# Kernel tuning notes

Measured on AMD Instinct MI355X. Metric: run time of the kernel, lower is better.

Reference implementation:

```python
import jax, jax.numpy as jnp
import numpy as np

B, T, H, IN, OUT = 256, 1024, 512, 2, 2


def setup_inputs() -> dict:
    key = jax.random.key(0)
    ks = jax.random.split(key, 12)
    s = 1.0 / np.sqrt(H)
    return {
        "X0": jax.random.normal(ks[0], (B, OUT), jnp.float32),
        "V": jax.random.normal(ks[1], (B, T, IN), jnp.float32),
        # GRU params (torch layout: gates ordered r, z, n)
        "W_ih": jax.random.uniform(ks[2], (3 * H, IN), jnp.float32, -s, s),
        "W_hh": jax.random.uniform(ks[3], (3 * H, H), jnp.float32, -s, s),
        "b_ih": jax.random.uniform(ks[4], (3 * H,), jnp.float32, -s, s),
        "b_hh": jax.random.uniform(ks[5], (3 * H,), jnp.float32, -s, s),
        # attention MLP: Linear(OUT+IN, H//2) -> ReLU -> Linear(H//2, OUT) -> Softmax
        "Wa1": jax.random.uniform(ks[6], (H // 2, OUT + IN), jnp.float32, -s, s),
        "ba1": jax.random.uniform(ks[7], (H // 2,), jnp.float32, -s, s),
        "Wa2": jax.random.uniform(ks[8], (OUT, H // 2), jnp.float32, -s, s),
        "ba2": jax.random.uniform(ks[9], (OUT,), jnp.float32, -s, s),
        # residual layer: Linear(H, OUT)
        "Wr": jax.random.uniform(ks[10], (OUT, H), jnp.float32, -s, s),
        "br": jax.random.uniform(ks[11], (OUT,), jnp.float32, -s, s),
    }


def _forward(X0, V, W_ih, W_hh, b_ih, b_hh, Wa1, ba1, Wa2, ba2, Wr, br):
    # ---- GRU over time (batch_first input, h0 = 0) ----
    # Precompute input projections for all steps: [B, T, 3H]
    gx_all = jnp.einsum('bti,gi->btg', V, W_ih) + b_ih
    gx_tm = jnp.swapaxes(gx_all, 0, 1)  # [T, B, 3H]

    def gru_step(h, gx):
        gh = h @ W_hh.T + b_hh  # [B, 3H]
        r = jax.nn.sigmoid(gx[:, :H] + gh[:, :H])
        z = jax.nn.sigmoid(gx[:, H:2 * H] + gh[:, H:2 * H])
        n = jnp.tanh(gx[:, 2 * H:] + r * gh[:, 2 * H:])
        h_new = (1.0 - z) * n + z * h
        return h_new, h_new

    h0 = jnp.zeros((V.shape[0], H), V.dtype)
    _, h_seq = jax.lax.scan(gru_step, h0, gx_tm)  # [T, B, H]

    # residual_raw = residual_layer(h_t), precomputed for all t: [T, B, OUT]
    res_all = jnp.einsum('tbh,oh->tbo', h_seq, Wr) + br

    v_tm = jnp.swapaxes(V, 0, 1)  # [T, B, IN]; IN == OUT so slice is identity

    def corr_step(x_prev, inp):
        v_t, res_t = inp
        att_in = jnp.concatenate([x_prev, v_t[:, :OUT]], axis=-1)  # [B, OUT+IN]
        hid = jax.nn.relu(att_in @ Wa1.T + ba1)
        aw = jax.nn.softmax(hid @ Wa2.T + ba2, axis=-1)  # [B, OUT]
        x_t = x_prev + v_t[:, :OUT] + aw * res_t
        return x_t, x_t

    _, x_seq = jax.lax.scan(corr_step, X0, (v_tm, res_all))  # [T, B, OUT]
    return jnp.swapaxes(x_seq, 0, 1)  # [B, T, OUT]


def reference(X0, V, W_ih, W_hh, b_ih, b_hh, Wa1, ba1, Wa2, ba2, Wr, br):
    return _forward(X0, V, W_ih, W_hh, b_ih, b_hh, Wa1, ba1, Wa2, ba2, Wr, br)
```

## Files before the change

kernel.cpp:

```cpp
#include <hip/hip_runtime.h>


typedef short bf16x8 __attribute__((ext_vector_type(8)));
typedef float f32x4  __attribute__((ext_vector_type(4)));
typedef unsigned u32x4 __attribute__((ext_vector_type(4)));

__device__ __forceinline__ unsigned f2bf(float f) {
  unsigned u = __builtin_bit_cast(unsigned, f);
  return (u + 0x7fffu + ((u >> 16) & 1u)) >> 16;
}

#define KSTEP(kt, areg) \
  acc0 = __builtin_amdgcn_mfma_f32_16x16x32_bf16(areg, wf0[kt], acc0, 0, 0, 0); \
  acc1 = __builtin_amdgcn_mfma_f32_16x16x32_bf16(areg, wf1[kt], acc1, 0, 0, 0); \
  acc2 = __builtin_amdgcn_mfma_f32_16x16x32_bf16(areg, wf2[kt], acc2, 0, 0, 0);

#define PUBU(off, val) \
  asm volatile("global_store_dwordx4 %0, %1, off offset:" #off " sc1" \
               :: "v"(pp), "v"(val) : "memory")

__global__ void __launch_bounds__(256, 1) gru_phase1(
    const float* __restrict__ V, const float* __restrict__ W_ih,
    const float* __restrict__ W_hh, const float* __restrict__ b_ih,
    const float* __restrict__ b_hh, const float* __restrict__ Wr,
    float* __restrict__ res_part,
    char* __restrict__ hbuf)
{
  const int tid  = threadIdx.x;
  const int w    = tid >> 6;
  const int lane = tid & 63;
  const int cl   = lane & 15;
  const int hi4  = lane >> 4;
  const int g    = blockIdx.x & 15;
  const int p    = (blockIdx.x >> 4) & 7;

  __shared__ short hs[2][16][512];
  __shared__ float rscratch[4][16][2];
  char* lds = (char*)hs;

  const int c = p * 64 + w * 16 + cl;

  const float wir0 = W_ih[c * 2 + 0],          wir1 = W_ih[c * 2 + 1];
  const float wiz0 = W_ih[(512 + c) * 2 + 0],  wiz1 = W_ih[(512 + c) * 2 + 1];
  const float win0 = W_ih[(1024 + c) * 2 + 0], win1 = W_ih[(1024 + c) * 2 + 1];
  const float bsr = b_ih[c] + b_hh[c];
  const float bsz = b_ih[512 + c] + b_hh[512 + c];
  const float bin = b_ih[1024 + c];
  const float bhn = b_hh[1024 + c];
  const float wr0 = Wr[c], wr1 = Wr[512 + c];

  bf16x8 wf0[16], wf1[16], wf2[16];
  #pragma unroll
  for (int gt = 0; gt < 3; ++gt) {
    const float* src = W_hh + ((size_t)(gt * 512 + c)) * 512 + hi4 * 8;
    #pragma unroll
    for (int kt = 0; kt < 16; ++kt) {
      float4 x = *reinterpret_cast<const float4*>(src + kt * 32);
      float4 y = *reinterpret_cast<const float4*>(src + kt * 32 + 4);
      bf16x8 t;
      t[0] = (short)f2bf(x.x); t[1] = (short)f2bf(x.y);
      t[2] = (short)f2bf(x.z); t[3] = (short)f2bf(x.w);
      t[4] = (short)f2bf(y.x); t[5] = (short)f2bf(y.y);
      t[6] = (short)f2bf(y.z); t[7] = (short)f2bf(y.w);
      if (gt == 0) wf0[kt] = t; else if (gt == 1) wf1[kt] = t; else wf2[kt] = t;
    }
  }

  for (int i = tid; i < 8192; i += 256) ((unsigned*)lds)[i] = 0;
  __syncthreads();

  const int urow = tid >> 4, ucol = tid & 15;
  const unsigned roff = (unsigned)(urow * 256 + ucol * 16);

  float h[4] = {0.f, 0.f, 0.f, 0.f};

  for (int s = 0; s < 1024; ++s) {
    float2 vv[4];
    #pragma unroll
    for (int j = 0; j < 4; ++j)
      vv[j] = *reinterpret_cast<const float2*>(
          &V[((size_t)(g * 16 + hi4 * 4 + j) * 1024 + (size_t)s) * 2]);

    f32x4 acc0 = {0.f,0.f,0.f,0.f}, acc1 = {0.f,0.f,0.f,0.f}, acc2 = {0.f,0.f,0.f,0.f};
    if (s > 0) {
      const char* ab = lds + (s & 1) * 16384 + cl * 1024;
      const unsigned sw = (unsigned)((cl & 7) << 4);
      #pragma unroll
      for (int kb = 0; kb < 4; ++kb) {
        bf16x8 a0 = *(const bf16x8*)(ab + (((kb * 4 + 0) * 64 + hi4 * 16) ^ sw));
        bf16x8 a1 = *(const bf16x8*)(ab + (((kb * 4 + 1) * 64 + hi4 * 16) ^ sw));
        bf16x8 a2 = *(const bf16x8*)(ab + (((kb * 4 + 2) * 64 + hi4 * 16) ^ sw));
        bf16x8 a3 = *(const bf16x8*)(ab + (((kb * 4 + 3) * 64 + hi4 * 16) ^ sw));
        KSTEP(kb * 4 + 0, a0) KSTEP(kb * 4 + 1, a1)
        KSTEP(kb * 4 + 2, a2) KSTEP(kb * 4 + 3, a3)
      }
    }

    float hn_[4];
    #pragma unroll
    for (int j = 0; j < 4; ++j) {
      float pr = acc0[j] + bsr + wir0 * vv[j].x + wir1 * vv[j].y;
      float pz = acc1[j] + bsz + wiz0 * vv[j].x + wiz1 * vv[j].y;
      float rg = 1.f / (1.f + __expf(-pr));
      float zg = 1.f / (1.f + __expf(-pz));
      float pn = win0 * vv[j].x + win1 * vv[j].y + bin + rg * (acc2[j] + bhn);
      pn = fminf(fmaxf(pn, -30.f), 30.f);
      float e2 = __expf(2.f * pn);
      float tg = (e2 - 1.f) / (e2 + 1.f);
      hn_[j] = (1.f - zg) * tg + zg * h[j];
      h[j] = hn_[j];
    }

    unsigned pk[4];
    #pragma unroll
    for (int j = 0; j < 4; ++j) {
      float o = __shfl_xor(hn_[j], 1);
      pk[j] = f2bf(hn_[j]) | (f2bf(o) << 16);
    }

    {
      unsigned q[4];
      #pragma unroll
      for (int j = 0; j < 4; ++j) q[j] = __shfl_xor(pk[j], 2);
      if (!(cl & 3)) {
        char* pp = hbuf + (size_t)(s & 1) * 524288 + (size_t)(g * 8 + p) * 4096
                 + (unsigned)(hi4 * 4) * 256u + (unsigned)((w * 16 + cl) >> 2) * 16u;
        u32x4 v0, v1, v2, v3;
        v0.x = pk[0]; v0.y = q[0]; v0.z = (unsigned)(s + 1); v0.w = 0u;
        v1.x = pk[1]; v1.y = q[1]; v1.z = (unsigned)(s + 1); v1.w = 0u;
        v2.x = pk[2]; v2.y = q[2]; v2.z = (unsigned)(s + 1); v2.w = 0u;
        v3.x = pk[3]; v3.y = q[3]; v3.z = (unsigned)(s + 1); v3.w = 0u;
        PUBU(0, v0); PUBU(256, v1); PUBU(512, v2); PUBU(768, v3);
      }
    }

    if (!(cl & 1)) {
      char* wb = lds + ((s + 1) & 1) * 16384;
      const unsigned bc = (unsigned)(2 * c);
      #pragma unroll
      for (int j = 0; j < 4; ++j) {
        const unsigned row = (unsigned)(hi4 * 4 + j);
        *(unsigned*)(wb + row * 1024 + (bc ^ ((row & 7) << 4))) = pk[j];
      }
    }

    {
      float p0[4], p1[4];
      #pragma unroll
      for (int j = 0; j < 4; ++j) { p0[j] = wr0 * hn_[j]; p1[j] = wr1 * hn_[j]; }
      #pragma unroll
      for (int m = 1; m < 16; m <<= 1) {
        #pragma unroll
        for (int j = 0; j < 4; ++j) {
          p0[j] += __shfl_xor(p0[j], m);
          p1[j] += __shfl_xor(p1[j], m);
        }
      }
      if (cl == 0) {
        #pragma unroll
        for (int j = 0; j < 4; ++j) {
          rscratch[w][hi4 * 4 + j][0] = p0[j];
          rscratch[w][hi4 * 4 + j][1] = p1[j];
        }
      }
    }
    __syncthreads();

    if (tid < 16) {
      float r0 = rscratch[0][tid][0] + rscratch[1][tid][0] +
                 rscratch[2][tid][0] + rscratch[3][tid][0];
      float r1 = rscratch[0][tid][1] + rscratch[1][tid][1] +
                 rscratch[2][tid][1] + rscratch[3][tid][1];
      float2 val; val.x = r0; val.y = r1;
      *reinterpret_cast<float2*>(
          &res_part[(((size_t)s * 256 + g * 16 + tid) * 8 + p) * 2]) = val;
    }

    if (s < 1023) {
      char* wb = lds + ((s + 1) & 1) * 16384;
      const unsigned want = (unsigned)(s + 1);
      const char* sbase = hbuf + (size_t)(s & 1) * 524288 + (size_t)(g * 8) * 4096 + roff;
      u32x4 u0, u1, u2, u3, u4, u5, u6;
      unsigned pend = 0x7f;
      #define RP(r) ((p + (r) + 1) & 7)
      #define ISSUE(r, ureg) \
        if (pend & (1u << (r))) { \
          const char* src = sbase + RP(r) * 4096; \
          asm volatile("global_load_dwordx4 %0, %1, off sc1" \
                       : "=v"(ureg) : "v"(src) : "memory"); \
        }
      #define HARVEST(r, ureg) \
        if ((pend & (1u << (r))) && ureg.z == want) { \
          const unsigned bc = (unsigned)(RP(r) * 128 + ucol * 8); \
          uint2 pay; pay.x = ureg.x; pay.y = ureg.y; \
          *(uint2*)(wb + (unsigned)urow * 1024 + \
                    (bc ^ (((unsigned)urow & 7) << 4))) = pay; \
          pend &= ~(1u << (r)); \
        }
      int gd = 0;
      while (pend) {
        ISSUE(0, u0) ISSUE(1, u1) ISSUE(2, u2) ISSUE(3, u3)
        ISSUE(4, u4) ISSUE(5, u5) ISSUE(6, u6)
        asm volatile("s_waitcnt vmcnt(0)" ::: "memory");
        HARVEST(0, u0) HARVEST(1, u1) HARVEST(2, u2) HARVEST(3, u3)
        HARVEST(4, u4) HARVEST(5, u5) HARVEST(6, u6)
        if (++gd > (1 << 14)) break;
      }
      #undef RP
      #undef ISSUE
      #undef HARVEST
    }
    __syncthreads();
  }
}

__global__ void __launch_bounds__(256) corr_phase2(
    const float* __restrict__ X0,
    const float* __restrict__ V,
    const float* __restrict__ Wa1,
    const float* __restrict__ ba1,
    const float* __restrict__ Wa2,
    const float* __restrict__ ba2,
    const float* __restrict__ br,
    const float* __restrict__ res_part,
    float* __restrict__ out)
{
  const int tid = threadIdx.x;
  const int wv = tid >> 6;
  const int lane = tid & 63;
  const int b = blockIdx.x * 4 + wv;

  float w1[4][4], bb1[4], w20[4], w21[4];
  #pragma unroll
  for (int q = 0; q < 4; q++) {
    const int h = lane * 4 + q;
    #pragma unroll
    for (int c = 0; c < 4; c++) w1[q][c] = Wa1[h * 4 + c];
    bb1[q] = ba1[h];
    w20[q] = Wa2[h];
    w21[q] = Wa2[256 + h];
  }
  const float c20 = ba2[0], c21 = ba2[1];
  const float br0 = br[0], br1 = br[1];
  float x0 = X0[b * 2], x1 = X0[b * 2 + 1];

  for (int c = 0; c < 16; c++) {
    const int tl = c * 64 + lane;
    const float2 vvl = *reinterpret_cast<const float2*>(&V[(b * 1024 + tl) * 2]);
    const float4* rp = reinterpret_cast<const float4*>(
        &res_part[((size_t)tl * 256 + b) * 16]);
    float4 q0 = rp[0], q1 = rp[1], q2 = rp[2], q3 = rp[3];
    float rr0 = (q0.x + q0.z) + (q1.x + q1.z) + (q2.x + q2.z) + (q3.x + q3.z);
    float rr1 = (q0.y + q0.w) + (q1.y + q1.w) + (q2.y + q2.w) + (q3.y + q3.w);
    float sx = 0.f, sy = 0.f;
    for (int k = 0; k < 64; k++) {
      const float v0 = __shfl(vvl.x, k);
      const float v1 = __shfl(vvl.y, k);
      const float r0 = __shfl(rr0, k) + br0;
      const float r1 = __shfl(rr1, k) + br1;
      float l0 = 0.f, l1 = 0.f;
      #pragma unroll
      for (int q = 0; q < 4; q++) {
        float hq = w1[q][0] * x0 + w1[q][1] * x1 + w1[q][2] * v0 + w1[q][3] * v1 + bb1[q];
        hq = fmaxf(hq, 0.f);
        l0 += w20[q] * hq;
        l1 += w21[q] * hq;
      }
      #pragma unroll
      for (int m = 1; m < 64; m <<= 1) {
        l0 += __shfl_xor(l0, m);
        l1 += __shfl_xor(l1, m);
      }
      l0 += c20; l1 += c21;
      const float mx = fmaxf(l0, l1);
      const float e0 = __expf(l0 - mx), e1 = __expf(l1 - mx);
      const float inv = 1.f / (e0 + e1);
      x0 += v0 + (e0 * inv) * r0;
      x1 += v1 + (e1 * inv) * r1;
      if (k == lane) { sx = x0; sy = x1; }
    }
    float2 o; o.x = sx; o.y = sy;
    *reinterpret_cast<float2*>(&out[(b * 1024 + c * 64 + lane) * 2]) = o;
  }
}

extern "C" void kernel_launch(void* const* d_in, const int* in_sizes, int n_in,
                              void* d_out, int out_size, void* d_ws, size_t ws_size,
                              hipStream_t stream) {
  const float* X0   = (const float*)d_in[0];
  const float* V    = (const float*)d_in[1];
  const float* W_ih = (const float*)d_in[2];
  const float* W_hh = (const float*)d_in[3];
  const float* b_ih = (const float*)d_in[4];
  const float* b_hh = (const float*)d_in[5];
  const float* Wa1  = (const float*)d_in[6];
  const float* ba1  = (const float*)d_in[7];
  const float* Wa2  = (const float*)d_in[8];
  const float* ba2  = (const float*)d_in[9];
  const float* Wr   = (const float*)d_in[10];
  const float* br   = (const float*)d_in[11];
  float* out = (float*)d_out;

  char* ws = (char*)d_ws;
  char*  hbuf     = ws;
  float* res_part = (float*)(ws + 1024 * 1024);
  hipMemsetAsync(hbuf, 0, 1024 * 1024, stream);

  hipLaunchKernelGGL(gru_phase1, dim3(128), dim3(256), 0, stream,
                     V, W_ih, W_hh, b_ih, b_hh, Wr, res_part, hbuf);
  hipLaunchKernelGGL(corr_phase2, dim3(64), dim3(256), 0, stream,
                     X0, V, Wa1, ba1, Wa2, ba2, br, res_part, out);
}
```

Measured before the change: 3.889 ms.

## Process two batch groups per GRU block and halve the grid

Each phase-1 block now handles two batch groups with the same register-resident W_hh slice, doubling LDS buffers and scratch, and launches 64 blocks instead of 128. Per-step compute and the two groups' global h exchanges are done back-to-back within one block. This aims to amortise the per-step barrier and latency overhead over more work and cut the number of polling blocks, at the cost of longer per-step critical path per block.

```diff
diff --git a/kernel.cpp b/kernel.cpp
--- a/kernel.cpp
+++ b/kernel.cpp
@@ -31,11 +31,12 @@
   const int lane = tid & 63;
   const int cl   = lane & 15;
   const int hi4  = lane >> 4;
-  const int g    = blockIdx.x & 15;
-  const int p    = (blockIdx.x >> 4) & 7;
-
-  __shared__ short hs[2][16][512];
-  __shared__ float rscratch[4][16][2];
+  const int pr_  = blockIdx.x & 7;
+  const int p    = blockIdx.x >> 3;
+  const int gA   = pr_ * 2, gB = gA + 1;
+
+  __shared__ short hs[2][2][16][512];
+  __shared__ float rsc[2][4][16][2];
   char* lds = (char*)hs;
 
   const int c = p * 64 + w * 16 + cl;
@@ -66,15 +67,16 @@
     }
   }
 
-  for (int i = tid; i < 8192; i += 256) ((unsigned*)lds)[i] = 0;
+  for (int i = tid; i < 16384; i += 256) ((unsigned*)lds)[i] = 0;
   __syncthreads();
 
   const int urow = tid >> 4, ucol = tid & 15;
   const unsigned roff = (unsigned)(urow * 256 + ucol * 16);
 
-  float h[4] = {0.f, 0.f, 0.f, 0.f};
-
-  for (int s = 0; s < 1024; ++s) {
+  float hA[4] = {0.f, 0.f, 0.f, 0.f};
+  float hB[4] = {0.f, 0.f, 0.f, 0.f};
+
+  auto process = [&](int s, int sub, int g, float* h) {
     float2 vv[4];
     #pragma unroll
     for (int j = 0; j < 4; ++j)
@@ -83,7 +85,7 @@
 
     f32x4 acc0 = {0.f,0.f,0.f,0.f}, acc1 = {0.f,0.f,0.f,0.f}, acc2 = {0.f,0.f,0.f,0.f};
     if (s > 0) {
-      const char* ab = lds + (s & 1) * 16384 + cl * 1024;
+      const char* ab = lds + (s & 1) * 32768 + sub * 16384 + cl * 1024;
       const unsigned sw = (unsigned)((cl & 7) << 4);
       #pragma unroll
       for (int kb = 0; kb < 4; ++kb) {
@@ -99,9 +101,9 @@
     float hn_[4];
     #pragma unroll
     for (int j = 0; j < 4; ++j) {
-      float pr = acc0[j] + bsr + wir0 * vv[j].x + wir1 * vv[j].y;
-      float pz = acc1[j] + bsz + wiz0 * vv[j].x + wiz1 * vv[j].y;
-      float rg = 1.f / (1.f + __expf(-pr));
+      float prr = acc0[j] + bsr + wir0 * vv[j].x + wir1 * vv[j].y;
+      float pz  = acc1[j] + bsz + wiz0 * vv[j].x + wiz1 * vv[j].y;
+      float rg = 1.f / (1.f + __expf(-prr));
       float zg = 1.f / (1.f + __expf(-pz));
       float pn = win0 * vv[j].x + win1 * vv[j].y + bin + rg * (acc2[j] + bhn);
       pn = fminf(fmaxf(pn, -30.f), 30.f);
@@ -135,7 +137,7 @@
     }
 
     if (!(cl & 1)) {
-      char* wb = lds + ((s + 1) & 1) * 16384;
+      char* wb = lds + ((s + 1) & 1) * 32768 + sub * 16384;
       const unsigned bc = (unsigned)(2 * c);
       #pragma unroll
       for (int j = 0; j < 4; ++j) {
@@ -159,56 +161,70 @@
       if (cl == 0) {
         #pragma unroll
         for (int j = 0; j < 4; ++j) {
-          rscratch[w][hi4 * 4 + j][0] = p0[j];
-          rscratch[w][hi4 * 4 + j][1] = p1[j];
+          rsc[sub][w][hi4 * 4 + j][0] = p0[j];
+          rsc[sub][w][hi4 * 4 + j][1] = p1[j];
         }
       }
     }
+  };
+
+  auto consume = [&](int s, int sub, int g) {
+    char* wb = lds + ((s + 1) & 1) * 32768 + sub * 16384;
+    const unsigned want = (unsigned)(s + 1);
+    const char* sbase = hbuf + (size_t)(s & 1) * 524288 + (size_t)(g * 8) * 4096 + roff;
+    u32x4 u0, u1, u2, u3, u4, u5, u6;
+    unsigned pend = 0x7f;
+    #define RP(r) ((p + (r) + 1) & 7)
+    #define ISSUE(r, ureg) \
+      if (pend & (1u << (r))) { \
+        const char* src = sbase + RP(r) * 4096; \
+        asm volatile("global_load_dwordx4 %0, %1, off sc1" \
+                     : "=v"(ureg) : "v"(src) : "memory"); \
+      }
+    #define HARVEST(r, ureg) \
+      if ((pend & (1u << (r))) && ureg.z == want) { \
+        const unsigned bc = (unsigned)(RP(r) * 128 + ucol * 8); \
+        uint2 pay; pay.x = ureg.x; pay.y = ureg.y; \
+        *(uint2*)(wb + (unsigned)urow * 1024 + \
+                  (bc ^ (((unsigned)urow & 7) << 4))) = pay; \
+        pend &= ~(1u << (r)); \
+      }
+    int gd = 0;
+    while (pend) {
+      ISSUE(0, u0) ISSUE(1, u1) ISSUE(2, u2) ISSUE(3, u3)
+      ISSUE(4, u4) ISSUE(5, u5) ISSUE(6, u6)
+      asm volatile("s_waitcnt vmcnt(0)" ::: "memory");
+      HARVEST(0, u0) HARVEST(1, u1) HARVEST(2, u2) HARVEST(3, u3)
+      HARVEST(4, u4) HARVEST(5, u5) HARVEST(6, u6)
+      if (++gd > (1 << 14)) break;
+    }
+    #undef RP
+    #undef ISSUE
+    #undef HARVEST
+  };
+
+  for (int s = 0; s < 1024; ++s) {
+    process(s, 0, gA, hA);
+    process(s, 1, gB, hB);
     __syncthreads();
 
     if (tid < 16) {
-      float r0 = rscratch[0][tid][0] + rscratch[1][tid][0] +
-                 rscratch[2][tid][0] + rscratch[3][tid][0];
-      float r1 = rscratch[0][tid][1] + rscratch[1][tid][1] +
-                 rscratch[2][tid][1] + rscratch[3][tid][1];
-      float2 val; val.x = r0; val.y = r1;
-      *reinterpret_cast<float2*>(
-          &res_part[(((size_t)s * 256 + g * 16 + tid) * 8 + p) * 2]) = val;
+      #pragma unroll
+      for (int sub = 0; sub < 2; ++sub) {
+        const int g = sub ? gB : gA;
+        float r0 = rsc[sub][0][tid][0] + rsc[sub][1][tid][0] +
+                   rsc[sub][2][tid][0] + rsc[sub][3][tid][0];
+        float r1 = rsc[sub][0][tid][1] + rsc[sub][1][tid][1] +
+                   rsc[sub][2][tid][1] + rsc[sub][3][tid][1];
+        float2 val; val.x = r0; val.y = r1;
+        *reinterpret_cast<float2*>(
+            &res_part[(((size_t)s * 256 + g * 16 + tid) * 8 + p) * 2]) = val;
+      }
     }
 
     if (s < 1023) {
-      char* wb = lds + ((s + 1) & 1) * 16384;
-      const unsigned want = (unsigned)(s + 1);
-      const char* sbase = hbuf + (size_t)(s & 1) * 524288 + (size_t)(g * 8) * 4096 + roff;
-      u32x4 u0, u1, u2, u3, u4, u5, u6;
-      unsigned pend = 0x7f;
-      #define RP(r) ((p + (r) + 1) & 7)
-      #define ISSUE(r, ureg) \
-        if (pend & (1u << (r))) { \
-          const char* src = sbase + RP(r) * 4096; \
-          asm volatile("global_load_dwordx4 %0, %1, off sc1" \
-                       : "=v"(ureg) : "v"(src) : "memory"); \
-        }
-      #define HARVEST(r, ureg) \
-        if ((pend & (1u << (r))) && ureg.z == want) { \
-          const unsigned bc = (unsigned)(RP(r) * 128 + ucol * 8); \
-          uint2 pay; pay.x = ureg.x; pay.y = ureg.y; \
-          *(uint2*)(wb + (unsigned)urow * 1024 + \
-                    (bc ^ (((unsigned)urow & 7) << 4))) = pay; \
-          pend &= ~(1u << (r)); \
-        }
-      int gd = 0;
-      while (pend) {
-        ISSUE(0, u0) ISSUE(1, u1) ISSUE(2, u2) ISSUE(3, u3)
-        ISSUE(4, u4) ISSUE(5, u5) ISSUE(6, u6)
-        asm volatile("s_waitcnt vmcnt(0)" ::: "memory");
-        HARVEST(0, u0) HARVEST(1, u1) HARVEST(2, u2) HARVEST(3, u3)
-        HARVEST(4, u4) HARVEST(5, u5) HARVEST(6, u6)
-        if (++gd > (1 << 14)) break;
-      }
-      #undef RP
-      #undef ISSUE
-      #undef HARVEST
+      consume(s, 0, gA);
+      consume(s, 1, gB);
     }
     __syncthreads();
   }
@@ -306,7 +322,7 @@
   float* res_part = (float*)(ws + 1024 * 1024);
   hipMemsetAsync(hbuf, 0, 1024 * 1024, stream);
 
-  hipLaunchKernelGGL(gru_phase1, dim3(128), dim3(256), 0, stream,
+  hipLaunchKernelGGL(gru_phase1, dim3(64), dim3(256), 0, stream,
                      V, W_ih, W_hh, b_ih, b_hh, Wr, res_part, hbuf);
   hipLaunchKernelGGL(corr_phase2, dim3(64), dim3(256), 0, stream,
                      X0, V, Wa1, ba1, Wa2, ba2, br, res_part, out);
```

New measurement: 6.240 ms. 1.6x slower.
